# Optimization experiments

Hardware: AMD Instinct MI355X
Metric: run time of the kernel (lower is better)

## Reference

```python
import jax, jax.numpy as jnp
import numpy as np

SCALING = 2.0  # lora scaling attached via set_lora (lora_alpha / r)


def setup_inputs() -> dict:
    key = jax.random.key(0)
    ks = jax.random.split(key, 8)
    E, DIN, DOUT, N, K, R = 8, 2048, 2048, 4096, 2, 16
    inputs = jax.random.normal(ks[0], (N, DIN), jnp.float32)
    weight = jax.random.normal(ks[1], (E, DOUT, DIN), jnp.float32) * 0.02
    lora_A = jax.random.normal(ks[2], (E, R, DIN), jnp.float32) * 0.02
    lora_B = jax.random.normal(ks[3], (E, DOUT, R), jnp.float32) * 0.02
    gates = jax.nn.softmax(jax.random.normal(ks[4], (N, K), jnp.float32), axis=-1)
    # expert assignment per (token, slot); scattermoe contract:
    #   sorted_scattered_idxs = argsort(assign); token = idx // k, slot = idx % k
    assign = jax.random.randint(ks[5], (N * K,), 0, E)
    sorted_scattered_idxs = jnp.argsort(assign).astype(jnp.int32)
    sorted_expert_idxs = assign[sorted_scattered_idxs].astype(jnp.int32)
    counts = jnp.bincount(assign, length=E)
    expert_offsets = jnp.cumsum(counts).astype(jnp.int32)
    return dict(inputs=inputs, weight=weight, lora_A=lora_A, lora_B=lora_B,
                gates=gates, sorted_expert_idxs=sorted_expert_idxs,
                sorted_scattered_idxs=sorted_scattered_idxs,
                expert_offsets=expert_offsets, k=K)


def reference(inputs, weight, lora_A, lora_B, gates, sorted_expert_idxs,
              sorted_scattered_idxs, expert_offsets, k):
    # Fused LoRA grouped GEMM:  Y = X @ W + scaling * (X @ A^T) @ B^T
    # grouped_in=False, grouped_out=False, bias=None (module defaults).
    E = weight.shape[0]
    N = gates.shape[0]
    W = jnp.swapaxes(weight, 1, 2)          # [E, din, dout] (weight.permute(0,2,1))
    token = sorted_scattered_idxs // k      # source token per sorted slot
    slot = sorted_scattered_idxs % k        # which of the k routes
    x = inputs[token]                       # gather -> [N*k, din]
    y = jnp.zeros((x.shape[0], W.shape[2]), x.dtype)
    for e in range(E):                      # fixed small expert loop
        m = (sorted_expert_idxs == e)[:, None]
        xe = jnp.where(m, x, 0.0)
        y = y + (xe @ W[e] + SCALING * ((xe @ jnp.swapaxes(lora_A[e], 0, 1)) @ jnp.swapaxes(lora_B[e], 0, 1)))
    g = gates[token, slot][:, None]         # gate per sorted slot
    out = jnp.zeros((N, W.shape[2]), y.dtype).at[token].add(y * g)
    return out
```

## Files before the change

kernel.cpp:

```cpp
#include <hip/hip_runtime.h>
#include <hip/hip_bf16.h>

#define E_    8
#define DIN   2048
#define DOUT  2048
#define N_TOK 4096
#define NK    8192
#define R_    16
#define KEXT  2112
#define KT_N  (KEXT / 64)
#define BM    256
#define BN    256
#define MT_MAX 40

typedef __bf16 bf16x8 __attribute__((ext_vector_type(8)));
typedef float  f32x4  __attribute__((ext_vector_type(4)));

static __device__ __forceinline__ void gld16(const void* g, void* l) {
  __builtin_amdgcn_global_load_lds(
      (const __attribute__((address_space(1))) unsigned int*)g,
      (__attribute__((address_space(3))) unsigned int*)l, 16, 0, 0);
}

static __device__ __forceinline__ unsigned short f2bfu(float f) {
  union { float f; unsigned int u; } v; v.f = f;
  unsigned int r = v.u + 0x7fffu + ((v.u >> 16) & 1u);
  return (unsigned short)(r >> 16);
}

__global__ void __launch_bounds__(256)
k_prep(const float* __restrict__ w, const float* __restrict__ lb,
       unsigned short* __restrict__ wbe,
       const float* __restrict__ la, unsigned short* __restrict__ Ab,
       const float* __restrict__ x, const int* __restrict__ ssi,
       const float* __restrict__ gates, const int* __restrict__ kptr,
       unsigned short* __restrict__ Xe, float* __restrict__ gate,
       int* __restrict__ tok) {
  const int b = blockIdx.x, tid = threadIdx.x;
  if (b < 4096) {
    const int wv = tid >> 6, ln = tid & 63;
    const long long row = ((long long)b << 2) | wv;
    const float4* src  = (const float4*)(w + row * DIN);
    const float4* lsrc = (const float4*)(lb + row * R_);
    ushort4* dst = (ushort4*)(wbe + row * KEXT);
    for (int u = ln; u < KEXT / 4; u += 64) {
      float4 v;
      if (u < 512)       v = src[u];
      else if (u < 516)  v = lsrc[u - 512];
      else               v = make_float4(0.f, 0.f, 0.f, 0.f);
      ushort4 o;
      o.x = f2bfu(v.x); o.y = f2bfu(v.y); o.z = f2bfu(v.z); o.w = f2bfu(v.w);
      dst[u] = o;
    }
  } else if (b < 12288) {
    const int s = b - 4096;
    int ssv = ssi[s];
    int kk = kptr[0];
    int t = ssv / kk, sl = ssv - t * kk;
    if (tid == 0) { gate[s] = gates[t * kk + sl]; tok[s] = t; }
    const float4* src = (const float4*)(x + (long long)t * DIN);
    ushort4* dst = (ushort4*)(Xe + (long long)s * KEXT);
    for (int i = tid; i < 512; i += 256) {
      float4 v = src[i];
      ushort4 o;
      o.x = f2bfu(v.x); o.y = f2bfu(v.y); o.z = f2bfu(v.z); o.w = f2bfu(v.w);
      dst[i] = o;
    }
    if (tid < 12) {
      ushort4 z; z.x = z.y = z.z = z.w = 0;
      dst[516 + tid] = z;
    }
  } else {
    const int i = ((b - 12288) << 8) + tid;
    float4 v = ((const float4*)la)[i];
    ushort4 o;
    o.x = f2bfu(v.x); o.y = f2bfu(v.y); o.z = f2bfu(v.z); o.w = f2bfu(v.w);
    ((ushort4*)Ab)[i] = o;
  }
}

__global__ void __launch_bounds__(256)
k_xa(unsigned short* __restrict__ Xe, const unsigned short* __restrict__ Ab,
     const int* __restrict__ eoff) {
  __shared__ f32x4 red[4][64];
  int tile = blockIdx.x;
  int off_prev = 0, e = -1, m_start = 0, m_end = 0, acc_t = 0;
#pragma unroll
  for (int i = 0; i < E_; i++) {
    int oe = eoff[i];
    int te = (oe - off_prev + 15) >> 4;
    if (e < 0 && tile < acc_t + te) {
      e = i; m_start = off_prev + (tile - acc_t) * 16; m_end = oe;
    }
    acc_t += te; off_prev = oe;
  }
  if (e < 0) return;
  const int tid = threadIdx.x;
  const int wv = tid >> 6, lane = tid & 63;
  const int l15 = lane & 15, quad = lane >> 4;
  int arow = m_start + l15; if (arow >= m_end) arow = m_end - 1;
  const unsigned short* xp = Xe + (long long)arow * KEXT + wv * 512 + quad * 8;
  const unsigned short* bp = Ab + ((long long)e * R_ + l15) * DIN + wv * 512 + quad * 8;
  f32x4 acc = (f32x4){0.f, 0.f, 0.f, 0.f};
#pragma unroll 8
  for (int k0 = 0; k0 < 512; k0 += 32) {
    bf16x8 a = *(const bf16x8*)(xp + k0);
    bf16x8 b = *(const bf16x8*)(bp + k0);
    acc = __builtin_amdgcn_mfma_f32_16x16x32_bf16(a, b, acc, 0, 0, 0);
  }
  red[wv][lane] = acc;
  __syncthreads();
  if (wv == 0) {
    f32x4 s = red[0][lane] + red[1][lane] + red[2][lane] + red[3][lane];
#pragma unroll
    for (int t = 0; t < 4; t++) {
      int slot = m_start + quad * 4 + t;
      if (slot < m_end)
        Xe[(long long)slot * KEXT + 2048 + l15] = f2bfu(2.0f * s[t]);
    }
  }
}

__global__ void __launch_bounds__(512, 2)
k_gemm(const unsigned short* __restrict__ Xe, const unsigned short* __restrict__ Wbe,
       const float* __restrict__ gate, const int* __restrict__ tok,
       const int* __restrict__ eoff, float* __restrict__ out) {
  __shared__ alignas(16) unsigned short sA[2][BM * 64];
  __shared__ alignas(16) unsigned short sB[2][BN * 64];
  __shared__ float gs[BM];
  __shared__ int   ts[BM];

  const int id  = blockIdx.x;
  const int nt  = id & 7;
  const int jb  = id >> 3;
  const int kh  = jb & 1;
  const int mt  = jb >> 1;
  const int n_start = nt << 8;

  int off_prev = 0, e = -1, m_start = 0, m_end = 0, acc_t = 0;
#pragma unroll
  for (int i = 0; i < E_; i++) {
    int oe = eoff[i];
    int te = (oe - off_prev + 255) >> 8;
    if (e < 0 && mt < acc_t + te) {
      e = i; m_start = off_prev + (mt - acc_t) * 256; m_end = oe;
    }
    acc_t += te;
    off_prev = oe;
  }
  if (e < 0) return;

  const int tid = threadIdx.x;
  const int w = tid >> 6, lane = tid & 63;
  const int wm = w >> 2, wn = w & 3;
  const int quad = lane >> 4, l15 = lane & 15;
  const int srow = lane >> 3;
  const int scol = ((lane & 7) ^ srow) * 8;

  if (tid < 256) {
    int gm = m_start + tid; if (gm >= m_end) gm = m_end - 1;
    gs[tid] = gate[gm];
    ts[tid] = tok[gm];
  }

  f32x4 acc[8][4];
#pragma unroll
  for (int mi = 0; mi < 8; mi++)
#pragma unroll
    for (int ni = 0; ni < 4; ni++)
      acc[mi][ni] = (f32x4){0.f, 0.f, 0.f, 0.f};

  const unsigned short* Wb = Wbe + (long long)e * DOUT * KEXT;

#define STAGE(buf, kt_)                                                              \
  {                                                                                  \
    const int k0s = (kt_) * 64;                                                      \
    _Pragma("unroll")                                                                \
    for (int jj = 0; jj < 4; jj++) {                                                 \
      const int c = (w << 2) + jj;                                                   \
      const int rt = (c << 3) + srow;                                                \
      int ga = m_start + rt; if (ga >= m_end) ga = m_end - 1;     \
      gld16(Xe + (long long)ga * KEXT + k0s + scol, &sA[buf][(c << 9) + (lane << 3)]); \
      gld16(Wb + (long long)(n_start + rt) * KEXT + k0s + scol,                      \
            &sB[buf][(c << 9) + (lane << 3)]);                                       \
    }                                                                                \
  }

  const int kt_beg = kh * 17;
  const int kt_end = kh ? KT_N : 17;

  asm volatile("s_waitcnt vmcnt(0) lgkmcnt(0)" ::: "memory");
  STAGE(0, kt_beg);

  for (int kt = kt_beg; kt < kt_end; ++kt) {
    const int b = (kt - kt_beg) & 1;
    if (kt + 1 < kt_end) {
      STAGE(b ^ 1, kt + 1);
      asm volatile("s_waitcnt vmcnt(8)" ::: "memory");
    } else {
      asm volatile("s_waitcnt vmcnt(0)" ::: "memory");
    }
    __builtin_amdgcn_s_barrier();
    __builtin_amdgcn_sched_barrier(0);
#pragma unroll
    for (int ks = 0; ks < 2; ks++) {
      const int kx = (((ks << 2) | quad) ^ (l15 & 7)) << 3;
      bf16x8 af[8], bfr[4];
#pragma unroll
      for (int mi = 0; mi < 8; mi++)
        af[mi] = *(const bf16x8*)&sA[b][(wm * 128 + mi * 16 + l15) * 64 + kx];
#pragma unroll
      for (int ni = 0; ni < 4; ni++)
        bfr[ni] = *(const bf16x8*)&sB[b][(wn * 64 + ni * 16 + l15) * 64 + kx];
#pragma unroll
      for (int mi = 0; mi < 8; mi++)
#pragma unroll
        for (int ni = 0; ni < 4; ni++)
          acc[mi][ni] = __builtin_amdgcn_mfma_f32_16x16x32_bf16(
              af[mi], bfr[ni], acc[mi][ni], 0, 0, 0);
    }
    asm volatile("" ::: "memory");
    __builtin_amdgcn_s_barrier();
    __builtin_amdgcn_sched_barrier(0);
  }
#undef STAGE

#pragma unroll
  for (int mi = 0; mi < 8; mi++) {
    const int rbase = wm * 128 + mi * 16 + quad * 4;
#pragma unroll
    for (int t4 = 0; t4 < 4; t4++) {
      const int row = rbase + t4;
      if (m_start + row >= m_end) continue;
      const float g = gs[row];
      float* orow = out + (long long)ts[row] * DOUT + n_start + wn * 64 + l15;
#pragma unroll
      for (int ni = 0; ni < 4; ni++)
        atomicAdd(orow + ni * 16, acc[mi][ni][t4] * g);
    }
  }
}

extern "C" void kernel_launch(void* const* d_in, const int* in_sizes, int n_in,
                              void* d_out, int out_size, void* d_ws, size_t ws_size,
                              hipStream_t stream) {
  (void)in_sizes; (void)n_in; (void)out_size; (void)ws_size;
  const float* inputs = (const float*)d_in[0];
  const float* weight = (const float*)d_in[1];
  const float* lora_A = (const float*)d_in[2];
  const float* lora_B = (const float*)d_in[3];
  const float* gates  = (const float*)d_in[4];
  const int* sei  = (const int*)d_in[5];
  const int* ssi  = (const int*)d_in[6];
  const int* eoff = (const int*)d_in[7];
  const int* kptr = (const int*)d_in[8];
  (void)sei;
  float* out = (float*)d_out;

  unsigned char* ws = (unsigned char*)d_ws;
  unsigned short* Wbe = (unsigned short*)ws;
  unsigned short* Xe  = (unsigned short*)(ws + 69206016);
  unsigned short* Ab  = (unsigned short*)(ws + 103809024);
  float* gate = (float*)(ws + 104333312);
  int*   tok  = (int*)(ws + 104366080);

  hipMemsetAsync(d_out, 0, (size_t)N_TOK * DOUT * sizeof(float), stream);
  k_prep<<<4096 + 8192 + 256, 256, 0, stream>>>(weight, lora_B, Wbe, lora_A, Ab,
                                                inputs, ssi, gates, kptr, Xe, gate, tok);
  k_xa<<<519, 256, 0, stream>>>(Xe, Ab, eoff);
  k_gemm<<<MT_MAX * 8 * 2, 512, 0, stream>>>(Xe, Wbe, gate, tok, eoff, out);
}
```

Before: 446.9 us.

## Drop split-K and interleave global prefetch with MFMA phases in grouped GEMM

Removes the two-way split-K decomposition so each block covers the full K range, halving the grid and the number of atomic adds into the output. The inner loop is restructured into four phases: each phase issues part of the next tile's global-to-LDS loads, reads a slice of A fragments, and runs MFMAs under raised wave priority. Barriers and vmcnt waits are set finely so memory traffic overlaps with compute. In exchange the grid is smaller, which may underfill CUs, and the denser barrier and wait schedule is fragile.

After: 454.5 us. No clear change (+1.7%).

```diff
diff --git a/kernel.cpp b/kernel.cpp
--- a/kernel.cpp
+++ b/kernel.cpp
@@ -132,9 +132,7 @@
 
   const int id  = blockIdx.x;
   const int nt  = id & 7;
-  const int jb  = id >> 3;
-  const int kh  = jb & 1;
-  const int mt  = jb >> 1;
+  const int mt  = id >> 3;
   const int n_start = nt << 8;
 
   int off_prev = 0, e = -1, m_start = 0, m_end = 0, acc_t = 0;
@@ -156,6 +154,8 @@
   const int quad = lane >> 4, l15 = lane & 15;
   const int srow = lane >> 3;
   const int scol = ((lane & 7) ^ srow) * 8;
+  const int kx0 = ((0 | quad) ^ (l15 & 7)) << 3;
+  const int kx1 = ((4 | quad) ^ (l15 & 7)) << 3;
 
   if (tid < 256) {
     int gm = m_start + tid; if (gm >= m_end) gm = m_end - 1;
@@ -172,58 +172,88 @@
 
   const unsigned short* Wb = Wbe + (long long)e * DOUT * KEXT;
 
-#define STAGE(buf, kt_)                                                              \
-  {                                                                                  \
-    const int k0s = (kt_) * 64;                                                      \
-    _Pragma("unroll")                                                                \
-    for (int jj = 0; jj < 4; jj++) {                                                 \
-      const int c = (w << 2) + jj;                                                   \
-      const int rt = (c << 3) + srow;                                                \
-      int ga = m_start + rt; if (ga >= m_end) ga = m_end - 1;     \
-      gld16(Xe + (long long)ga * KEXT + k0s + scol, &sA[buf][(c << 9) + (lane << 3)]); \
-      gld16(Wb + (long long)(n_start + rt) * KEXT + k0s + scol,                      \
-            &sB[buf][(c << 9) + (lane << 3)]);                                       \
-    }                                                                                \
-  }
-
-  const int kt_beg = kh * 17;
-  const int kt_end = kh ? KT_N : 17;
+#define SWEEP(buf_, kt_, s_)                                                        \
+  do {                                                                              \
+    const int k0s_ = (kt_) * 64;                                                    \
+    if ((s_) < 4) {                                                                 \
+      const int c_ = ((s_) << 3) + w;                                               \
+      const int rt_ = (c_ << 3) + srow;                                             \
+      gld16(Wb + (long long)(n_start + rt_) * KEXT + k0s_ + scol,                   \
+            &sB[buf_][(c_ << 9) + (lane << 3)]);                                    \
+    } else {                                                                        \
+      const int cb_ = (((s_) - 4) & 1) * 16 + ((((s_) - 4) >> 1) & 1) * 8;          \
+      const int c_ = cb_ + w;                                                       \
+      const int rt_ = (c_ << 3) + srow;                                             \
+      int ga_ = m_start + rt_; if (ga_ >= m_end) ga_ = m_end - 1;                   \
+      gld16(Xe + (long long)ga_ * KEXT + k0s_ + scol,                               \
+            &sA[buf_][(c_ << 9) + (lane << 3)]);                                    \
+    }                                                                               \
+  } while (0)
+
+#define PHASE(p_)                                                                   \
+  {                                                                                 \
+    _Pragma("unroll")                                                               \
+    for (int dm = 0; dm < 2; dm++) {                                                \
+      const int row_ = (wm * 128 + ((p_) * 2 + dm) * 16 + l15) * 64;                \
+      af[dm * 2 + 0] = *(const bf16x8*)&sA[b][row_ + kx0];                          \
+      af[dm * 2 + 1] = *(const bf16x8*)&sA[b][row_ + kx1];                          \
+    }                                                                               \
+    asm volatile("s_waitcnt lgkmcnt(0)" ::: "memory");                              \
+    __builtin_amdgcn_sched_barrier(0);                                              \
+    __builtin_amdgcn_s_setprio(1);                                                  \
+    _Pragma("unroll")                                                               \
+    for (int dm = 0; dm < 2; dm++)                                                  \
+      _Pragma("unroll")                                                             \
+      for (int ni = 0; ni < 4; ni++) {                                              \
+        acc[(p_) * 2 + dm][ni] = __builtin_amdgcn_mfma_f32_16x16x32_bf16(           \
+            af[dm * 2 + 0], bfr[ni * 2 + 0], acc[(p_) * 2 + dm][ni], 0, 0, 0);      \
+        acc[(p_) * 2 + dm][ni] = __builtin_amdgcn_mfma_f32_16x16x32_bf16(           \
+            af[dm * 2 + 1], bfr[ni * 2 + 1], acc[(p_) * 2 + dm][ni], 0, 0, 0);      \
+      }                                                                             \
+    __builtin_amdgcn_s_setprio(0);                                                  \
+  }
 
   asm volatile("s_waitcnt vmcnt(0) lgkmcnt(0)" ::: "memory");
-  STAGE(0, kt_beg);
-
-  for (int kt = kt_beg; kt < kt_end; ++kt) {
-    const int b = (kt - kt_beg) & 1;
-    if (kt + 1 < kt_end) {
-      STAGE(b ^ 1, kt + 1);
-      asm volatile("s_waitcnt vmcnt(8)" ::: "memory");
-    } else {
-      asm volatile("s_waitcnt vmcnt(0)" ::: "memory");
-    }
+  SWEEP(0, 0, 0); SWEEP(0, 0, 1); SWEEP(0, 0, 2); SWEEP(0, 0, 3);
+  SWEEP(0, 0, 4); SWEEP(0, 0, 5); SWEEP(0, 0, 6); SWEEP(0, 0, 7);
+
+  for (int kt = 0; kt < KT_N; ++kt) {
+    const int b = kt & 1, nb = b ^ 1;
+    const bool more = (kt + 1 < KT_N);
+    bf16x8 af[4], bfr[8];
+
+    if (more) asm volatile("s_waitcnt vmcnt(2)" ::: "memory");
+    else      asm volatile("s_waitcnt vmcnt(0)" ::: "memory");
     __builtin_amdgcn_s_barrier();
     __builtin_amdgcn_sched_barrier(0);
-#pragma unroll
-    for (int ks = 0; ks < 2; ks++) {
-      const int kx = (((ks << 2) | quad) ^ (l15 & 7)) << 3;
-      bf16x8 af[8], bfr[4];
-#pragma unroll
-      for (int mi = 0; mi < 8; mi++)
-        af[mi] = *(const bf16x8*)&sA[b][(wm * 128 + mi * 16 + l15) * 64 + kx];
-#pragma unroll
-      for (int ni = 0; ni < 4; ni++)
-        bfr[ni] = *(const bf16x8*)&sB[b][(wn * 64 + ni * 16 + l15) * 64 + kx];
-#pragma unroll
-      for (int mi = 0; mi < 8; mi++)
-#pragma unroll
-        for (int ni = 0; ni < 4; ni++)
-          acc[mi][ni] = __builtin_amdgcn_mfma_f32_16x16x32_bf16(
-              af[mi], bfr[ni], acc[mi][ni], 0, 0, 0);
-    }
-    asm volatile("" ::: "memory");
+    if (more) { SWEEP(nb, kt + 1, 0); SWEEP(nb, kt + 1, 1); }
+#pragma unroll
+    for (int ni = 0; ni < 4; ni++) {
+      const int brow_ = (wn * 64 + ni * 16 + l15) * 64;
+      bfr[ni * 2 + 0] = *(const bf16x8*)&sB[b][brow_ + kx0];
+      bfr[ni * 2 + 1] = *(const bf16x8*)&sB[b][brow_ + kx1];
+    }
+    PHASE(0)
+
     __builtin_amdgcn_s_barrier();
     __builtin_amdgcn_sched_barrier(0);
-  }
-#undef STAGE
+    if (more) { SWEEP(nb, kt + 1, 2); SWEEP(nb, kt + 1, 3); }
+    PHASE(1)
+
+    if (more) asm volatile("s_waitcnt vmcnt(4)" ::: "memory");
+    else      asm volatile("s_waitcnt vmcnt(0)" ::: "memory");
+    __builtin_amdgcn_s_barrier();
+    __builtin_amdgcn_sched_barrier(0);
+    if (more) { SWEEP(nb, kt + 1, 4); SWEEP(nb, kt + 1, 5); }
+    PHASE(2)
+
+    __builtin_amdgcn_s_barrier();
+    __builtin_amdgcn_sched_barrier(0);
+    if (more) { SWEEP(nb, kt + 1, 6); SWEEP(nb, kt + 1, 7); }
+    PHASE(3)
+  }
+#undef SWEEP
+#undef PHASE
 
 #pragma unroll
   for (int mi = 0; mi < 8; mi++) {
@@ -268,5 +298,5 @@
   k_prep<<<4096 + 8192 + 256, 256, 0, stream>>>(weight, lora_B, Wbe, lora_A, Ab,
                                                 inputs, ssi, gates, kptr, Xe, gate, tok);
   k_xa<<<519, 256, 0, stream>>>(Xe, Ab, eoff);
-  k_gemm<<<MT_MAX * 8 * 2, 512, 0, stream>>>(Xe, Wbe, gate, tok, eoff, out);
-}
+  k_gemm<<<MT_MAX * 8, 512, 0, stream>>>(Xe, Wbe, gate, tok, eoff, out);
+}
```
